# Performance work log

Measured on AMD Instinct MI355X. Metric: run time of the kernel, lower is better.

The kernel has to match this reference:

```python
import jax, jax.numpy as jnp
import numpy as np

D_MODEL = 1024
N_DIM = 64      # per-head dim; scores scaled by 1/sqrt(n_dim)
N_HEADS = 16
SEQ = 4096
LN_EPS = 1e-5


def setup_inputs() -> dict:
    key = jax.random.key(0)
    ks = jax.random.split(key, 12)
    hd = N_HEADS * N_DIM  # == D_MODEL (required by residual add)
    s = 0.02
    return {
        "embed_word_vec": jax.random.normal(ks[0], (SEQ, D_MODEL), dtype=jnp.float32),
        "attn_mask": jax.random.uniform(ks[1], (SEQ, SEQ)) < 0.1,  # True = masked out
        "wq": jax.random.normal(ks[2], (D_MODEL, hd), dtype=jnp.float32) * s,
        "bq": jnp.zeros((hd,), dtype=jnp.float32),
        "wk": jax.random.normal(ks[3], (D_MODEL, hd), dtype=jnp.float32) * s,
        "bk": jnp.zeros((hd,), dtype=jnp.float32),
        "wv": jax.random.normal(ks[4], (D_MODEL, hd), dtype=jnp.float32) * s,
        "bv": jnp.zeros((hd,), dtype=jnp.float32),
        "wo": jax.random.normal(ks[5], (hd, D_MODEL), dtype=jnp.float32) * s,
        "bo": jnp.zeros((D_MODEL,), dtype=jnp.float32),
        "gamma": jnp.ones((D_MODEL,), dtype=jnp.float32),
        "beta": jnp.zeros((D_MODEL,), dtype=jnp.float32),
    }


def reference(embed_word_vec, attn_mask, wq, bq, wk, bk, wv, bv, wo, bo, gamma, beta):
    x = embed_word_vec                      # [S, d_model]
    q = x @ wq + bq                         # [S, H*D]
    k = x @ wk + bk
    v = x @ wv + bv
    scores = (q @ k.T) / jnp.sqrt(jnp.asarray(N_DIM, dtype=q.dtype))  # [S, S]
    scores = jnp.where(attn_mask, jnp.asarray(-jnp.inf, dtype=scores.dtype), scores)
    attention = jax.nn.softmax(scores, axis=-1)                       # [S, S]
    context = attention @ v + x             # AV + residual, [S, d_model]
    h = context @ wo + bo                   # out projection
    # LayerNorm over last dim
    mu = jnp.mean(h, axis=-1, keepdims=True)
    var = jnp.mean(jnp.square(h - mu), axis=-1, keepdims=True)
    output = (h - mu) * jax.lax.rsqrt(var + LN_EPS) * gamma + beta
    return (output, attention)
```

## Files before the change

### kernel.cpp

```cpp
#include <hip/hip_runtime.h>
#include <hip/hip_bf16.h>
#include <stdint.h>

#define SEQ 4096
#define DM  1024

typedef __attribute__((ext_vector_type(8))) short bf16x8;
typedef __attribute__((ext_vector_type(4))) float f32x4;

template <int V> struct Int { static constexpr int v = V; };

__device__ __forceinline__ short f2bf(float f) {
  union { float f; unsigned int i; } x; x.f = f;
  unsigned int r = x.i + 0x7FFFu + ((x.i >> 16) & 1u);
  return (short)(r >> 16);
}
__device__ __forceinline__ float bf2f(short s) {
  union { unsigned int i; float f; } u;
  u.i = ((unsigned int)(unsigned short)s) << 16;
  return u.f;
}

__device__ __forceinline__ void gload16(const short* g, short* l) {
  __builtin_amdgcn_global_load_lds(
      (const __attribute__((address_space(1))) unsigned int*)g,
      (__attribute__((address_space(3))) unsigned int*)l, 16, 0, 0);
}

__device__ __forceinline__ float wave_max(float v) {
#pragma unroll
  for (int o = 32; o; o >>= 1) v = fmaxf(v, __shfl_xor(v, o));
  return v;
}
__device__ __forceinline__ float wave_sum(float v) {
#pragma unroll
  for (int o = 32; o; o >>= 1) v += __shfl_xor(v, o);
  return v;
}

#define BARRIER() do { asm volatile("" ::: "memory"); \
  __builtin_amdgcn_s_barrier(); asm volatile("" ::: "memory"); } while (0)
#define MF(a, b, c) __builtin_amdgcn_mfma_f32_16x16x32_bf16(a, b, c, 0, 0, 0)

template <int EPI>
__global__ __launch_bounds__(512, 2) void gemm8(
    const short* __restrict__ A, const short* __restrict__ B,
    short* __restrict__ C, short* __restrict__ Cv,
    const float* __restrict__ bias, int Ksplit, int lda, int ldb, int ldc,
    int ldv, float scale, int ntm, int ntn, long csplit, int pc) {
  __shared__ short lds[2][4][8192];
  const int tid = threadIdx.x;
  const int lane = tid & 63;
  const int wid = tid >> 6;
  const int wr = wid >> 2;
  const int wc = wid & 3;
  const int bid = blockIdx.x, nwg = gridDim.x;
  const int chunk = nwg >> 3;
  const int wl = (bid & 7) * chunk + (bid >> 3);
  const int tpg = ntm * ntn;
  const int split = wl / tpg;
  const int r0 = wl - split * tpg;
  const int q = r0 / chunk, i0 = r0 % chunk;
  const int npatch = ntn / pc;
  const int m0 = ((q / npatch) * (chunk / pc) + i0 / pc) * 256;
  const int n0 = ((q % npatch) * pc + i0 % pc) * 256;
  const short* Ab = A + (long)split * Ksplit;
  const short* Bb = B + (long)split * Ksplit;
  short* Co = C + (long)split * csplit;

  const int o0 = tid * 16;
  const int oo = o0 ^ (((o0 >> 7) & 7) << 4);
  const int sr0 = oo >> 7;
  const int sc0 = (oo & 127) >> 1;

  auto stA = [&](int buf, int h, int kt) {
    const short* g = Ab + (long)(m0 + h * 128 + sr0) * lda + kt * 64 + sc0;
    short* l = &lds[buf][h][0] + wid * 512;
    gload16(g, l);
    gload16(g + (long)64 * lda, l + 4096);
  };
  auto stB = [&](int buf, int h, int kt) {
    const short* g = Bb + (long)(n0 + h * 128 + sr0) * ldb + kt * 64 + sc0;
    short* l = &lds[buf][2 + h][0] + wid * 512;
    gload16(g, l);
    gload16(g + (long)64 * ldb, l + 4096);
  };

  const int ll = lane & 15, lh = lane >> 4;
  auto ldaf = [&](int buf, int c, int mm, int kk) {
    const int r = c * 32 + mm * 16 + ll;
    const int off = (r * 64 + kk * 32 + lh * 8) ^ ((r & 7) << 3);
    return *(const bf16x8*)(&lds[buf][wr][0] + off);
  };
  auto ldbf = [&](int buf, int n, int kk) {
    const int r = (wc & 1) * 64 + n * 16 + ll;
    const int off = (r * 64 + kk * 32 + lh * 8) ^ ((r & 7) << 3);
    return *(const bf16x8*)(&lds[buf][2 + (wc >> 1)][0] + off);
  };

  f32x4 acc[8][4];
#pragma unroll
  for (int i = 0; i < 8; i++)
#pragma unroll
    for (int j = 0; j < 4; j++) acc[i][j] = (f32x4){0.f, 0.f, 0.f, 0.f};
  bf16x8 Bf[4][2];

  const int NT = Ksplit >> 6;
  stB(0, 0, 0); stB(0, 1, 0);
  stA(0, 0, 0); stA(0, 1, 0);
  stB(1, 0, 1); stB(1, 1, 1);
  asm volatile("s_waitcnt vmcnt(4)" ::: "memory");
  BARRIER();

  auto phase = [&](auto BUF, auto CC, auto LB, auto BARv, auto&& stg) {
    constexpr int buf = decltype(BUF)::v;
    constexpr int c = decltype(CC)::v;
    if constexpr (decltype(LB)::v != 0) {
#pragma unroll
      for (int n = 0; n < 4; n++) {
        Bf[n][0] = ldbf(buf, n, 0);
        Bf[n][1] = ldbf(buf, n, 1);
      }
    }
    bf16x8 a00 = ldaf(buf, c, 0, 0), a01 = ldaf(buf, c, 0, 1);
    bf16x8 a10 = ldaf(buf, c, 1, 0), a11 = ldaf(buf, c, 1, 1);
    stg();
    if constexpr (decltype(BARv)::v != 0) BARRIER();
    __builtin_amdgcn_s_setprio(1);
#pragma unroll
    for (int n = 0; n < 4; n++) {
      acc[2 * c][n] = MF(a00, Bf[n][0], acc[2 * c][n]);
      acc[2 * c][n] = MF(a01, Bf[n][1], acc[2 * c][n]);
      acc[2 * c + 1][n] = MF(a10, Bf[n][0], acc[2 * c + 1][n]);
      acc[2 * c + 1][n] = MF(a11, Bf[n][1], acc[2 * c + 1][n]);
    }
    __builtin_amdgcn_s_setprio(0);
  };

  for (int t = 0; t < NT; t += 2) {
    const bool nl = (t + 2 < NT);
    phase(Int<0>{}, Int<0>{}, Int<1>{}, Int<0>{},
          [&] { stA(1, 0, t + 1); stA(1, 1, t + 1); });
    phase(Int<0>{}, Int<1>{}, Int<0>{}, Int<1>{}, [] {});
    phase(Int<0>{}, Int<2>{}, Int<0>{}, Int<0>{},
          [&] { if (nl) { stB(0, 0, t + 2); stB(0, 1, t + 2); } });
    phase(Int<0>{}, Int<3>{}, Int<0>{}, Int<0>{}, [] {});
    if (nl) { asm volatile("s_waitcnt vmcnt(4)" ::: "memory"); }
    else    { asm volatile("s_waitcnt vmcnt(0)" ::: "memory"); }
    BARRIER();
    phase(Int<1>{}, Int<0>{}, Int<1>{}, Int<0>{},
          [&] { if (nl) { stA(0, 0, t + 2); stA(0, 1, t + 2); } });
    phase(Int<1>{}, Int<1>{}, Int<0>{}, Int<1>{}, [] {});
    phase(Int<1>{}, Int<2>{}, Int<0>{}, Int<0>{},
          [&] { if (nl) { stB(1, 0, t + 3); stB(1, 1, t + 3); } });
    phase(Int<1>{}, Int<3>{}, Int<0>{}, Int<0>{}, [] {});
    if (nl) {
      asm volatile("s_waitcnt vmcnt(4)" ::: "memory");
      BARRIER();
    }
  }

  const int rb = m0 + wr * 128 + lh * 4;
  const int cb0 = n0 + wc * 64 + ll;
  if (EPI == 3 && n0 >= 2048) {
#pragma unroll
    for (int mi = 0; mi < 8; mi++) {
#pragma unroll
      for (int n = 0; n < 4; n++) {
        const int col = cb0 + n * 16;
        const float bv = bias[col];
        short4 pk;
        pk.x = f2bf(acc[mi][n][0] + bv);
        pk.y = f2bf(acc[mi][n][1] + bv);
        pk.z = f2bf(acc[mi][n][2] + bv);
        pk.w = f2bf(acc[mi][n][3] + bv);
        *(short4*)(Cv + (long)(col - 2048) * ldv + rb + mi * 16) = pk;
      }
    }
    return;
  }
#pragma unroll
  for (int mi = 0; mi < 8; mi++) {
#pragma unroll
    for (int n = 0; n < 4; n++) {
      const int col = cb0 + n * 16;
      float bv = 0.f;
      if (EPI == 1 || EPI == 3) bv = bias[col];
#pragma unroll
      for (int r = 0; r < 4; r++) {
        const int row = rb + mi * 16 + r;
        const long off = (long)row * ldc + col;
        float v = acc[mi][n][r];
        if (EPI == 1 || EPI == 3) v += bv;
        if (EPI == 2) v *= scale;
        Co[off] = f2bf(v);
      }
    }
  }
}


__global__ __launch_bounds__(256) void cvt_f32_to_bf16(
    const float* __restrict__ in, short* __restrict__ out, int n4) {
  int i = blockIdx.x * 256 + threadIdx.x;
  if (i < n4) {
    float4 f = ((const float4*)in)[i];
    short4 o;
    o.x = f2bf(f.x); o.y = f2bf(f.y); o.z = f2bf(f.z); o.w = f2bf(f.w);
    ((short4*)out)[i] = o;
  }
}

__global__ void transpose_w4(const float* __restrict__ s0,
                             const float* __restrict__ s1,
                             const float* __restrict__ s2,
                             const float* __restrict__ s3,
                             short* __restrict__ d0, short* __restrict__ d1,
                             short* __restrict__ d2, short* __restrict__ d3) {
  const int z = blockIdx.z;
  const float* in = z == 0 ? s0 : z == 1 ? s1 : z == 2 ? s2 : s3;
  short* out = z == 0 ? d0 : z == 1 ? d1 : z == 2 ? d2 : d3;
  __shared__ float tile[32][33];
  const int bx = blockIdx.x * 32;
  const int by = blockIdx.y * 32;
  const int tx = threadIdx.x, ty = threadIdx.y;
#pragma unroll
  for (int i = 0; i < 32; i += 8)
    tile[ty + i][tx] = in[(long)(by + ty + i) * 1024 + bx + tx];
  __syncthreads();
#pragma unroll
  for (int i = 0; i < 32; i += 8)
    out[(long)(bx + ty + i) * 1024 + by + tx] = f2bf(tile[tx][ty + i]);
}

__global__ __launch_bounds__(256) void concat_bias(
    const float* __restrict__ bq, const float* __restrict__ bk,
    const float* __restrict__ bv, float* __restrict__ o) {
  int i = blockIdx.x * 256 + threadIdx.x;
  float v = (i < 1024) ? bq[i] : (i < 2048 ? bk[i - 1024] : bv[i - 2048]);
  o[i] = v;
}

template <int FUSED>
__global__ __launch_bounds__(256) void softmax_rows(const short* __restrict__ Sb,
                                                    const int* __restrict__ mask,
                                                    short* __restrict__ Pb,
                                                    float* __restrict__ Af,
                                                    int ld) {
  const long row = blockIdx.x;
  const bf16x8* src = (const bf16x8*)(Sb + row * ld);
  const int* mrow = mask + row * (long)SEQ;
  bf16x8* dst = (bf16x8*)(Pb + row * SEQ);
  const int tid = threadIdx.x;
  const int wid = tid >> 6, lane = tid & 63;
  bf16x8 a = src[tid], b = src[tid + 256];
  int4 ma0 = *(const int4*)(mrow + tid * 8);
  int4 ma1 = *(const int4*)(mrow + tid * 8 + 4);
  int4 mb0 = *(const int4*)(mrow + 2048 + tid * 8);
  int4 mb1 = *(const int4*)(mrow + 2048 + tid * 8 + 4);
  float v[16];
#pragma unroll
  for (int j = 0; j < 8; j++) { v[j] = bf2f(a[j]); v[8 + j] = bf2f(b[j]); }
  const int* mm0 = (const int*)&ma0;
  const int* mm1 = (const int*)&ma1;
  const int* mm2 = (const int*)&mb0;
  const int* mm3 = (const int*)&mb1;
#pragma unroll
  for (int j = 0; j < 4; j++) {
    if (mm0[j]) v[j] = -INFINITY;
    if (mm1[j]) v[4 + j] = -INFINITY;
    if (mm2[j]) v[8 + j] = -INFINITY;
    if (mm3[j]) v[12 + j] = -INFINITY;
  }
  float mx = -INFINITY;
#pragma unroll
  for (int j = 0; j < 16; j++) mx = fmaxf(mx, v[j]);
  mx = wave_max(mx);
  __shared__ float red[4];
  if (lane == 0) red[wid] = mx;
  __syncthreads();
  mx = fmaxf(fmaxf(red[0], red[1]), fmaxf(red[2], red[3]));
  float sum = 0.f;
#pragma unroll
  for (int j = 0; j < 16; j++) {
    v[j] = __expf(v[j] - mx);
    sum += v[j];
  }
  sum = wave_sum(sum);
  __shared__ float red2[4];
  if (lane == 0) red2[wid] = sum;
  __syncthreads();
  sum = red2[0] + red2[1] + red2[2] + red2[3];
  const float inv = 1.0f / sum;
  bf16x8 o0, o1;
#pragma unroll
  for (int j = 0; j < 8; j++) {
    v[j] *= inv;
    v[8 + j] *= inv;
    o0[j] = f2bf(v[j]);
    o1[j] = f2bf(v[8 + j]);
  }
  dst[tid] = o0;
  dst[tid + 256] = o1;
  if (FUSED) {
    float* orow = Af + row * (long)SEQ;
    *(float4*)(orow + tid * 8) = (float4){v[0], v[1], v[2], v[3]};
    *(float4*)(orow + tid * 8 + 4) = (float4){v[4], v[5], v[6], v[7]};
    *(float4*)(orow + 2048 + tid * 8) = (float4){v[8], v[9], v[10], v[11]};
    *(float4*)(orow + 2048 + tid * 8 + 4) = (float4){v[12], v[13], v[14], v[15]};
  }
}

__global__ __launch_bounds__(256) void expand_bf16_f32(
    const short* __restrict__ in, float* __restrict__ out) {
  long i = (long)blockIdx.x * 256 + threadIdx.x;
  bf16x8 a = ((const bf16x8*)in)[i];
  float4 lo, hi;
  lo.x = bf2f(a[0]); lo.y = bf2f(a[1]); lo.z = bf2f(a[2]); lo.w = bf2f(a[3]);
  hi.x = bf2f(a[4]); hi.y = bf2f(a[5]); hi.z = bf2f(a[6]); hi.w = bf2f(a[7]);
  ((float4*)out)[2 * i] = lo;
  ((float4*)out)[2 * i + 1] = hi;
}

__global__ __launch_bounds__(256) void reduce_ctx4(
    const short* __restrict__ p, const float* __restrict__ x,
    short* __restrict__ cb) {
  const long i = (long)blockIdx.x * 256 + threadIdx.x;
  bf16x8 a = ((const bf16x8*)p)[i];
  bf16x8 b = ((const bf16x8*)(p + 4194304))[i];
  bf16x8 c = ((const bf16x8*)(p + 8388608))[i];
  bf16x8 d = ((const bf16x8*)(p + 12582912))[i];
  float4 x0 = ((const float4*)x)[2 * i];
  float4 x1 = ((const float4*)x)[2 * i + 1];
  float xs[8] = {x0.x, x0.y, x0.z, x0.w, x1.x, x1.y, x1.z, x1.w};
  bf16x8 o;
#pragma unroll
  for (int j = 0; j < 8; j++)
    o[j] = f2bf(bf2f(a[j]) + bf2f(b[j]) + bf2f(c[j]) + bf2f(d[j]) + xs[j]);
  ((bf16x8*)cb)[i] = o;
}

__global__ __launch_bounds__(256) void ln4(
    const short* __restrict__ ph, const float* __restrict__ bo,
    const float* __restrict__ gamma, const float* __restrict__ beta,
    float* __restrict__ out) {
  const long row = blockIdx.x;
  const int tid = threadIdx.x;
  const int wid = tid >> 6, lane = tid & 63;
  const long base = row * DM + tid * 4;
  short4 p0 = *(const short4*)(ph + base);
  short4 p1 = *(const short4*)(ph + 4194304 + base);
  short4 p2 = *(const short4*)(ph + 8388608 + base);
  short4 p3 = *(const short4*)(ph + 12582912 + base);
  float4 bb = *(const float4*)(bo + tid * 4);
  float v[4];
  v[0] = bf2f(p0.x) + bf2f(p1.x) + bf2f(p2.x) + bf2f(p3.x) + bb.x;
  v[1] = bf2f(p0.y) + bf2f(p1.y) + bf2f(p2.y) + bf2f(p3.y) + bb.y;
  v[2] = bf2f(p0.z) + bf2f(p1.z) + bf2f(p2.z) + bf2f(p3.z) + bb.z;
  v[3] = bf2f(p0.w) + bf2f(p1.w) + bf2f(p2.w) + bf2f(p3.w) + bb.w;
  float s = v[0] + v[1] + v[2] + v[3];
  s = wave_sum(s);
  __shared__ float red[4];
  if (lane == 0) red[wid] = s;
  __syncthreads();
  const float mu = (red[0] + red[1] + red[2] + red[3]) * (1.f / DM);
  float var = 0.f;
#pragma unroll
  for (int j = 0; j < 4; j++) {
    float d = v[j] - mu;
    var += d * d;
  }
  var = wave_sum(var);
  __shared__ float red2[4];
  if (lane == 0) red2[wid] = var;
  __syncthreads();
  var = (red2[0] + red2[1] + red2[2] + red2[3]) * (1.f / DM);
  const float inv = rsqrtf(var + 1e-5f);
  float4 g = *(const float4*)(gamma + tid * 4);
  float4 be = *(const float4*)(beta + tid * 4);
  float4 o;
  o.x = (v[0] - mu) * inv * g.x + be.x;
  o.y = (v[1] - mu) * inv * g.y + be.y;
  o.z = (v[2] - mu) * inv * g.z + be.z;
  o.w = (v[3] - mu) * inv * g.w + be.w;
  *(float4*)(out + base) = o;
}

extern "C" void kernel_launch(void* const* d_in, const int* in_sizes, int n_in,
                              void* d_out, int out_size, void* d_ws,
                              size_t ws_size, hipStream_t stream) {
  const float* x    = (const float*)d_in[0];
  const int* mask   = (const int*)d_in[1];
  const float* wq   = (const float*)d_in[2];
  const float* bq   = (const float*)d_in[3];
  const float* wk   = (const float*)d_in[4];
  const float* bk   = (const float*)d_in[5];
  const float* wv   = (const float*)d_in[6];
  const float* bv   = (const float*)d_in[7];
  const float* wo   = (const float*)d_in[8];
  const float* bo   = (const float*)d_in[9];
  const float* gamma = (const float*)d_in[10];
  const float* beta  = (const float*)d_in[11];

  float* out  = (float*)d_out;
  float* attn = out + 4194304;
  short* cbuf = (short*)out;

  char* w = (char*)d_ws;
  const bool fused = ws_size >= (size_t)83886080 + 16384;
  short* Sb   = fused ? (short*)attn + 4096 : (short*)attn;
  const int ldS = fused ? 8192 : 4096;
  short* pav  = fused ? (short*)(w + 50331648) : (short*)attn;
  short* phh  = fused ? pav : (short*)(attn + 8388608);
  float* bqkv = fused ? (float*)(w + 83886080) : (float*)(w + 50331648);

  short* wqkvT = (short*)(w + 0);
  short* woT   = (short*)(w + 6291456);
  short* xb    = (short*)(w + 8388608);
  short* qkv   = (short*)(w + 16777216);
  short* attnb = (short*)(w + 8388608);
  short* vT    = (short*)(w + 41943040);

  cvt_f32_to_bf16<<<4096, 256, 0, stream>>>(x, xb, 1048576);
  transpose_w4<<<dim3(32, 32, 4), dim3(32, 8), 0, stream>>>(
      wq, wk, wv, wo, wqkvT, wqkvT + 1048576, wqkvT + 2097152, woT);
  concat_bias<<<12, 256, 0, stream>>>(bq, bk, bv, bqkv);

  gemm8<3><<<192, 512, 0, stream>>>(xb, wqkvT, qkv, vT, bqkv,
                                    1024, 1024, 1024, 3072, 4096, 1.f,
                                    16, 12, 0, 6);

  gemm8<2><<<256, 512, 0, stream>>>(qkv, qkv + 1024, Sb, nullptr, nullptr,
                                    1024, 3072, 3072, ldS, 0, 0.125f,
                                    16, 16, 0, 8);

  if (fused)
    softmax_rows<1><<<SEQ, 256, 0, stream>>>(Sb, mask, attnb, attn, ldS);
  else
    softmax_rows<0><<<SEQ, 256, 0, stream>>>(Sb, mask, attnb, attn, ldS);

  gemm8<0><<<256, 512, 0, stream>>>(attnb, vT, pav, nullptr, nullptr,
                                    1024, 4096, 4096, 1024, 0, 1.f,
                                    16, 4, 4194304L, 4);

  reduce_ctx4<<<2048, 256, 0, stream>>>(pav, x, cbuf);

  gemm8<0><<<256, 512, 0, stream>>>(cbuf, woT, phh, nullptr, nullptr,
                                    256, 1024, 1024, 1024, 0, 1.f,
                                    16, 4, 4194304L, 4);

  ln4<<<SEQ, 256, 0, stream>>>(phh, bo, gamma, beta, out);

  if (!fused) expand_bf16_f32<<<8192, 256, 0, stream>>>(attnb, attn);
}
```

Before: 195.5 us.

## Triple-buffer A tiles and restructure GEMM main loop for deeper prefetch

```diff
diff --git a/kernel.cpp b/kernel.cpp
--- a/kernel.cpp
+++ b/kernel.cpp
@@ -48,7 +48,8 @@
     short* __restrict__ C, short* __restrict__ Cv,
     const float* __restrict__ bias, int Ksplit, int lda, int ldb, int ldc,
     int ldv, float scale, int ntm, int ntn, long csplit, int pc) {
-  __shared__ short lds[2][4][8192];
+  __shared__ short ldsA[3][2][8192];
+  __shared__ short ldsB[2][2][8192];
   const int tid = threadIdx.x;
   const int lane = tid & 63;
   const int wid = tid >> 6;
@@ -75,13 +76,13 @@
 
   auto stA = [&](int buf, int h, int kt) {
     const short* g = Ab + (long)(m0 + h * 128 + sr0) * lda + kt * 64 + sc0;
-    short* l = &lds[buf][h][0] + wid * 512;
+    short* l = &ldsA[buf][h][0] + wid * 512;
     gload16(g, l);
     gload16(g + (long)64 * lda, l + 4096);
   };
   auto stB = [&](int buf, int h, int kt) {
     const short* g = Bb + (long)(n0 + h * 128 + sr0) * ldb + kt * 64 + sc0;
-    short* l = &lds[buf][2 + h][0] + wid * 512;
+    short* l = &ldsB[buf][h][0] + wid * 512;
     gload16(g, l);
     gload16(g + (long)64 * ldb, l + 4096);
   };
@@ -90,12 +91,12 @@
   auto ldaf = [&](int buf, int c, int mm, int kk) {
     const int r = c * 32 + mm * 16 + ll;
     const int off = (r * 64 + kk * 32 + lh * 8) ^ ((r & 7) << 3);
-    return *(const bf16x8*)(&lds[buf][wr][0] + off);
+    return *(const bf16x8*)(&ldsA[buf][wr][0] + off);
   };
   auto ldbf = [&](int buf, int n, int kk) {
     const int r = (wc & 1) * 64 + n * 16 + ll;
     const int off = (r * 64 + kk * 32 + lh * 8) ^ ((r & 7) << 3);
-    return *(const bf16x8*)(&lds[buf][2 + (wc >> 1)][0] + off);
+    return *(const bf16x8*)(&ldsB[buf][wc >> 1][0] + off);
   };
 
   f32x4 acc[8][4];
@@ -106,26 +107,16 @@
   bf16x8 Bf[4][2];
 
   const int NT = Ksplit >> 6;
-  stB(0, 0, 0); stB(0, 1, 0);
-  stA(0, 0, 0); stA(0, 1, 0);
-  stB(1, 0, 1); stB(1, 1, 1);
-  asm volatile("s_waitcnt vmcnt(4)" ::: "memory");
+  stA(0, 0, 0); stA(0, 1, 0); stB(0, 0, 0); stB(0, 1, 0);
+  stA(1, 0, 1); stA(1, 1, 1); stB(1, 0, 1); stB(1, 1, 1);
+  asm volatile("s_waitcnt vmcnt(8)" ::: "memory");
   BARRIER();
 
-  auto phase = [&](auto BUF, auto CC, auto LB, auto BARv, auto&& stg) {
-    constexpr int buf = decltype(BUF)::v;
+  auto phase = [&](auto CC, int abuf, auto&& stg, bool bar) {
     constexpr int c = decltype(CC)::v;
-    if constexpr (decltype(LB)::v != 0) {
-#pragma unroll
-      for (int n = 0; n < 4; n++) {
-        Bf[n][0] = ldbf(buf, n, 0);
-        Bf[n][1] = ldbf(buf, n, 1);
-      }
-    }
-    bf16x8 a00 = ldaf(buf, c, 0, 0), a01 = ldaf(buf, c, 0, 1);
-    bf16x8 a10 = ldaf(buf, c, 1, 0), a11 = ldaf(buf, c, 1, 1);
+    bf16x8 a00 = ldaf(abuf, c, 0, 0), a01 = ldaf(abuf, c, 0, 1);
+    bf16x8 a10 = ldaf(abuf, c, 1, 0), a11 = ldaf(abuf, c, 1, 1);
     stg();
-    if constexpr (decltype(BARv)::v != 0) BARRIER();
     __builtin_amdgcn_s_setprio(1);
 #pragma unroll
     for (int n = 0; n < 4; n++) {
@@ -135,29 +126,31 @@
       acc[2 * c + 1][n] = MF(a11, Bf[n][1], acc[2 * c + 1][n]);
     }
     __builtin_amdgcn_s_setprio(0);
+    if (bar) BARRIER();
   };
 
-  for (int t = 0; t < NT; t += 2) {
-    const bool nl = (t + 2 < NT);
-    phase(Int<0>{}, Int<0>{}, Int<1>{}, Int<0>{},
-          [&] { stA(1, 0, t + 1); stA(1, 1, t + 1); });
-    phase(Int<0>{}, Int<1>{}, Int<0>{}, Int<1>{}, [] {});
-    phase(Int<0>{}, Int<2>{}, Int<0>{}, Int<0>{},
-          [&] { if (nl) { stB(0, 0, t + 2); stB(0, 1, t + 2); } });
-    phase(Int<0>{}, Int<3>{}, Int<0>{}, Int<0>{}, [] {});
-    if (nl) { asm volatile("s_waitcnt vmcnt(4)" ::: "memory"); }
-    else    { asm volatile("s_waitcnt vmcnt(0)" ::: "memory"); }
-    BARRIER();
-    phase(Int<1>{}, Int<0>{}, Int<1>{}, Int<0>{},
-          [&] { if (nl) { stA(0, 0, t + 2); stA(0, 1, t + 2); } });
-    phase(Int<1>{}, Int<1>{}, Int<0>{}, Int<1>{}, [] {});
-    phase(Int<1>{}, Int<2>{}, Int<0>{}, Int<0>{},
-          [&] { if (nl) { stB(1, 0, t + 3); stB(1, 1, t + 3); } });
-    phase(Int<1>{}, Int<3>{}, Int<0>{}, Int<0>{}, [] {});
-    if (nl) {
-      asm volatile("s_waitcnt vmcnt(4)" ::: "memory");
+  int a3 = 0;
+  for (int t = 0; t < NT; ++t) {
+    const int b2 = t & 1;
+    int an = a3 - 1; if (an < 0) an = 2;
+    const bool st = (t + 2 < NT);
+    const bool last = (t == NT - 1);
+#pragma unroll
+    for (int n = 0; n < 4; n++) {
+      Bf[n][0] = ldbf(b2, n, 0);
+      Bf[n][1] = ldbf(b2, n, 1);
+    }
+    phase(Int<0>{}, a3,
+          [&] { if (st) { stA(an, 0, t + 2); stA(an, 1, t + 2); } }, true);
+    phase(Int<1>{}, a3, [&] { if (st) stB(b2, 0, t + 2); }, false);
+    phase(Int<2>{}, a3, [&] { if (st) stB(b2, 1, t + 2); }, false);
+    phase(Int<3>{}, a3, [&] {}, false);
+    if (!last) {
+      if (st) { asm volatile("s_waitcnt vmcnt(8)" ::: "memory"); }
+      else    { asm volatile("s_waitcnt vmcnt(0)" ::: "memory"); }
       BARRIER();
     }
+    a3 = (a3 + 1 == 3) ? 0 : a3 + 1;
   }
 
   const int rb = m0 + wr * 128 + lh * 4;
```

New measurement: 196.9 us. No clear change (+0.7%).
